# Kernel optimization log

Hardware: AMD Instinct MI355X
Metric: run time of the kernel (lower is better)

## Reference

```python
import jax, jax.numpy as jnp
import numpy as np
import math

FILTER_SIZE = 11
FILTER_SIGMA = 1.5
C1 = 0.01 ** 2
C2 = 0.03 ** 2
PAD = FILTER_SIZE // 2


def _make_gauss_kernel(sigma, kernel_size, channel=3):
    mean = np.floor(0.5 * kernel_size)
    x = np.arange(kernel_size, dtype=np.float64)
    k1d = np.exp(-((x - mean) ** 2) / (2 * sigma ** 2)) * (1.0 / (2 * math.pi * sigma ** 2))
    k2d = np.outer(k1d, k1d).astype(np.float32)
    k2d = k2d / k2d.sum()
    # OIHW depthwise kernel: [channel, 1, k, k]
    return np.broadcast_to(k2d[None, None], (channel, 1, kernel_size, kernel_size)).copy()


def _depthwise_blur(x, kernel):
    # x: [B, 3, H, W], kernel: [3, 1, k, k]; groups=3, SAME padding (k//2)
    return jax.lax.conv_general_dilated(
        x, kernel,
        window_strides=(1, 1),
        padding=[(PAD, PAD), (PAD, PAD)],
        dimension_numbers=('NCHW', 'OIHW', 'NCHW'),
        feature_group_count=3,
    )


def setup_inputs() -> dict:
    key = jax.random.key(0)
    k1, k2 = jax.random.split(key)
    B, C, H, W = 32, 3, 512, 512
    image1 = jax.random.uniform(k1, (B, C, H, W), dtype=jnp.float32)
    image2 = jax.random.uniform(k2, (B, C, H, W), dtype=jnp.float32)
    gauss_kernel = jnp.asarray(_make_gauss_kernel(FILTER_SIGMA, FILTER_SIZE, channel=3))
    return {"image1": image1, "image2": image2, "gauss_kernel": gauss_kernel}


def reference(image1, image2, gauss_kernel):
    mu1 = _depthwise_blur(image1, gauss_kernel)
    mu2 = _depthwise_blur(image2, gauss_kernel)
    mu1_sq = mu1 * mu1
    mu2_sq = mu2 * mu2
    mu1_mu2 = mu1 * mu2
    sig1_sq = _depthwise_blur(image1 * image1, gauss_kernel) - mu1_sq
    sig2_sq = _depthwise_blur(image2 * image2, gauss_kernel) - mu2_sq
    sig1_sig2 = _depthwise_blur(image1 * image2, gauss_kernel) - mu1_mu2
    ssim_num = (2.0 * mu1_mu2 + C1) * (2.0 * sig1_sig2 + C2)
    ssim_den = (mu1_sq + mu2_sq + C1) * (sig1_sq + sig2_sq + C2)
    ssim_map = ssim_num / ssim_den
    dssim_map = (1.0 - ssim_map) * 0.5
    return dssim_map.mean()  # size_average=True
```

## Files before the change

kernel.cpp:

```cpp
#include <hip/hip_runtime.h>
#include <math.h>


namespace {
constexpr int IMG = 512;
constexpr int TW = 32;
constexpr int RB = 32;
constexpr int RING = RB + 10;
constexpr int SLOT = 44;
constexpr int XGN = TW / 8;
constexpr int SEGR = 128;
constexpr int NCHUNK = SEGR / RB;
constexpr int SEGN = IMG / SEGR;
constexpr int CTILES = IMG / TW;
constexpr int NIMG = 96;
constexpr float C1c = 1e-4f;
constexpr float C2c = 9e-4f;
constexpr float INV_N = 1.0f / 25165824.0f;
}

typedef float v2f __attribute__((ext_vector_type(2)));

__global__ void dssim_zero(float* ws) { ws[0] = 0.0f; }

__global__ void dssim_final(const float* __restrict__ ws, float* __restrict__ out) {
  out[0] = ws[0] * INV_N;
}

__global__ __launch_bounds__(256, 4) void dssim_main(
    const float* __restrict__ im1, const float* __restrict__ im2,
    const float* __restrict__ gk, float* __restrict__ ws)
{
  __shared__ float sR[XGN * RING * SLOT];

  const int tid = threadIdx.x;
  const int bid = blockIdx.x;
  const int img = bid >> 6;
  const int rem = bid & 63;
  const int tsx = rem & 15;
  const int seg = rem >> 4;
  const int X0s = tsx * TW;
  const int Y0  = seg * SEGR;

  const float* __restrict__ p1 = im1 + (size_t)img * (IMG * IMG);
  const float* __restrict__ p2 = im2 + (size_t)img * (IMG * IMG);

  float wt[11];
  {
    float ic = 1.0f / sqrtf(gk[5 * 11 + 5]);
    #pragma unroll
    for (int i = 0; i < 11; ++i) wt[i] = gk[i * 11 + 5] * ic;
  }
  v2f wp[12];
  #pragma unroll
  for (int m = 0; m < 12; ++m) {
    float lo = (m <= 10) ? wt[m] : 0.f;
    float hi = (m >= 1) ? wt[m - 1] : 0.f;
    wp[m].x = lo; wp[m].y = hi;
  }

  const int c   = tid & 31;
  const int yg  = tid >> 5;
  const int xg3 = c >> 3;
  const int cl  = c & 7;

  float lsum = 0.f;

  for (int kc = 0; kc < NCHUNK; ++kc) {
    const int r0    = (kc == 0) ? -5 : RB * kc + 5;
    const int ntask = (kc == 0) ? 8 * RING : 8 * RB;
    for (int t = tid; t < ntask; t += 256) {
      const int colsub = t & 7;
      const int dr  = t >> 3;
      const int rl  = r0 + dr;
      const int ry  = Y0 + rl;
      const int rr  = (rl + 5) % RING;
      const int xg  = colsub >> 1;
      const int sub = colsub & 1;
      const int cbs = X0s + xg * 8 + sub * 4 - 8;

      float a20[20], b20[20];
      if ((unsigned)ry < (unsigned)IMG) {
        const float* row1 = p1 + (size_t)ry * IMG;
        const float* row2 = p2 + (size_t)ry * IMG;
        if (cbs >= 0 && cbs + 20 <= IMG) {
          #pragma unroll
          for (int i = 0; i < 5; ++i) {
            float4 v1 = *(const float4*)(row1 + cbs + 4 * i);
            float4 v2 = *(const float4*)(row2 + cbs + 4 * i);
            a20[4*i+0] = v1.x; a20[4*i+1] = v1.y; a20[4*i+2] = v1.z; a20[4*i+3] = v1.w;
            b20[4*i+0] = v2.x; b20[4*i+1] = v2.y; b20[4*i+2] = v2.z; b20[4*i+3] = v2.w;
          }
        } else {
          #pragma unroll
          for (int e = 0; e < 20; ++e) {
            int cc = cbs + e;
            bool ok = (unsigned)cc < (unsigned)IMG;
            a20[e] = ok ? row1[cc] : 0.f;
            b20[e] = ok ? row2[cc] : 0.f;
          }
        }
      } else {
        #pragma unroll
        for (int e = 0; e < 20; ++e) { a20[e] = 0.f; b20[e] = 0.f; }
      }

      v2f o0[2], o1[2], o2[2], o3[2], o4[2];
      #pragma unroll
      for (int jp = 0; jp < 2; ++jp) {
        o0[jp] = 0.f; o1[jp] = 0.f; o2[jp] = 0.f; o3[jp] = 0.f; o4[jp] = 0.f;
      }
      #pragma unroll
      for (int i = 3; i <= 16; ++i) {
        float va = a20[i], vb = b20[i];
        float pa = va * va, pb = vb * vb, pab = va * vb;
        v2f va2; va2.x = va; va2.y = va;
        v2f vb2; vb2.x = vb; vb2.y = vb;
        v2f pa2; pa2.x = pa; pa2.y = pa;
        v2f pb2; pb2.x = pb; pb2.y = pb;
        v2f pc2; pc2.x = pab; pc2.y = pab;
        if (i - 3 < 12) {
          v2f w = wp[i - 3];
          o0[0] = __builtin_elementwise_fma(w, va2, o0[0]);
          o1[0] = __builtin_elementwise_fma(w, vb2, o1[0]);
          o2[0] = __builtin_elementwise_fma(w, pa2, o2[0]);
          o3[0] = __builtin_elementwise_fma(w, pb2, o3[0]);
          o4[0] = __builtin_elementwise_fma(w, pc2, o4[0]);
        }
        if (i - 5 >= 0) {
          v2f w = wp[i - 5];
          o0[1] = __builtin_elementwise_fma(w, va2, o0[1]);
          o1[1] = __builtin_elementwise_fma(w, vb2, o1[1]);
          o2[1] = __builtin_elementwise_fma(w, pa2, o2[1]);
          o3[1] = __builtin_elementwise_fma(w, pb2, o3[1]);
          o4[1] = __builtin_elementwise_fma(w, pc2, o4[1]);
        }
      }

      const int base  = (xg * RING + rr) * SLOT;
      const int jbase = base + 16 * sub;
      *(float4*)&sR[jbase]      = make_float4(o0[0].x, o1[0].x, o2[0].x, o3[0].x);
      *(float4*)&sR[jbase + 4]  = make_float4(o0[0].y, o1[0].y, o2[0].y, o3[0].y);
      *(float4*)&sR[jbase + 8]  = make_float4(o0[1].x, o1[1].x, o2[1].x, o3[1].x);
      *(float4*)&sR[jbase + 12] = make_float4(o0[1].y, o1[1].y, o2[1].y, o3[1].y);
      *(float4*)&sR[base + 32 + 4 * sub] =
          make_float4(o4[0].x, o4[0].y, o4[1].x, o4[1].y);
    }
    __syncthreads();

    v2f m1p[2], m2p[2], e11p[2], e22p[2], e12p[2];
    #pragma unroll
    for (int jp = 0; jp < 2; ++jp) {
      m1p[jp] = 0.f; m2p[jp] = 0.f; e11p[jp] = 0.f; e22p[jp] = 0.f; e12p[jp] = 0.f;
    }

    const int y0l = RB * kc + yg * 4;
    int idx = y0l % RING;
    #pragma unroll
    for (int rr = 0; rr < 14; ++rr) {
      const int a = (xg3 * RING + idx) * SLOT;
      float4 v4 = *(const float4*)&sR[a + 4 * cl];
      float  v5 = sR[a + 32 + cl];
      v2f x1; x1.x = v4.x; x1.y = v4.x;
      v2f x2; x2.x = v4.y; x2.y = v4.y;
      v2f x3; x3.x = v4.z; x3.y = v4.z;
      v2f x4; x4.x = v4.w; x4.y = v4.w;
      v2f x5; x5.x = v5;   x5.y = v5;
      if (rr < 12) {
        v2f w = wp[rr];
        m1p[0]  = __builtin_elementwise_fma(w, x1, m1p[0]);
        m2p[0]  = __builtin_elementwise_fma(w, x2, m2p[0]);
        e11p[0] = __builtin_elementwise_fma(w, x3, e11p[0]);
        e22p[0] = __builtin_elementwise_fma(w, x4, e22p[0]);
        e12p[0] = __builtin_elementwise_fma(w, x5, e12p[0]);
      }
      if (rr >= 2) {
        v2f w = wp[rr - 2];
        m1p[1]  = __builtin_elementwise_fma(w, x1, m1p[1]);
        m2p[1]  = __builtin_elementwise_fma(w, x2, m2p[1]);
        e11p[1] = __builtin_elementwise_fma(w, x3, e11p[1]);
        e22p[1] = __builtin_elementwise_fma(w, x4, e22p[1]);
        e12p[1] = __builtin_elementwise_fma(w, x5, e12p[1]);
      }
      idx++; if (idx == RING) idx = 0;
    }

    #pragma unroll
    for (int jp = 0; jp < 2; ++jp) {
      v2f m1 = m1p[jp], m2 = m2p[jp];
      v2f m1s = m1 * m1, m2s = m2 * m2, m12 = m1 * m2;
      v2f s11 = e11p[jp] - m1s, s22 = e22p[jp] - m2s, s12 = e12p[jp] - m12;
      v2f num = (2.f * m12 + C1c) * (2.f * s12 + C2c);
      v2f den = (m1s + m2s + C1c) * (s11 + s22 + C2c);
      lsum += (1.f - num.x * __builtin_amdgcn_rcpf(den.x)) * 0.5f;
      lsum += (1.f - num.y * __builtin_amdgcn_rcpf(den.y)) * 0.5f;
    }
    __syncthreads();
  }

  #pragma unroll
  for (int off = 32; off > 0; off >>= 1) lsum += __shfl_down(lsum, off);
  if ((tid & 63) == 0) sR[tid >> 6] = lsum;
  __syncthreads();
  if (tid == 0) atomicAdd(ws, sR[0] + sR[1] + sR[2] + sR[3]);
}

extern "C" void kernel_launch(void* const* d_in, const int* in_sizes, int n_in,
                              void* d_out, int out_size, void* d_ws, size_t ws_size,
                              hipStream_t stream) {
  const float* im1 = (const float*)d_in[0];
  const float* im2 = (const float*)d_in[1];
  const float* gk  = (const float*)d_in[2];
  float* out = (float*)d_out;
  float* ws  = (float*)d_ws;

  hipLaunchKernelGGL(dssim_zero, dim3(1), dim3(1), 0, stream, ws);
  hipLaunchKernelGGL(dssim_main, dim3(NIMG * CTILES * SEGN), dim3(256), 0, stream,
                     im1, im2, gk, ws);
  hipLaunchKernelGGL(dssim_final, dim3(1), dim3(1), 0, stream, ws, out);
}
```

Measured before the change: 284.5 us.

## Merge squared-moment blurs into one channel and swizzle shared-memory slots

```diff
diff --git a/kernel.cpp b/kernel.cpp
--- a/kernel.cpp
+++ b/kernel.cpp
@@ -7,7 +7,7 @@
 constexpr int TW = 32;
 constexpr int RB = 32;
 constexpr int RING = RB + 10;
-constexpr int SLOT = 44;
+constexpr int SLOT = 40;
 constexpr int XGN = TW / 8;
 constexpr int SEGR = 128;
 constexpr int NCHUNK = SEGR / RB;
@@ -105,82 +105,80 @@
         for (int e = 0; e < 20; ++e) { a20[e] = 0.f; b20[e] = 0.f; }
       }
 
-      v2f o0[2], o1[2], o2[2], o3[2], o4[2];
+      v2f o0[2], o1[2], oS[2], oX[2];
       #pragma unroll
       for (int jp = 0; jp < 2; ++jp) {
-        o0[jp] = 0.f; o1[jp] = 0.f; o2[jp] = 0.f; o3[jp] = 0.f; o4[jp] = 0.f;
+        o0[jp] = 0.f; o1[jp] = 0.f; oS[jp] = 0.f; oX[jp] = 0.f;
       }
       #pragma unroll
       for (int i = 3; i <= 16; ++i) {
         float va = a20[i], vb = b20[i];
-        float pa = va * va, pb = vb * vb, pab = va * vb;
+        float px = va * vb;
+        float ps = va * va + vb * vb;
         v2f va2; va2.x = va; va2.y = va;
         v2f vb2; vb2.x = vb; vb2.y = vb;
-        v2f pa2; pa2.x = pa; pa2.y = pa;
-        v2f pb2; pb2.x = pb; pb2.y = pb;
-        v2f pc2; pc2.x = pab; pc2.y = pab;
+        v2f ps2; ps2.x = ps; ps2.y = ps;
+        v2f px2; px2.x = px; px2.y = px;
         if (i - 3 < 12) {
           v2f w = wp[i - 3];
           o0[0] = __builtin_elementwise_fma(w, va2, o0[0]);
           o1[0] = __builtin_elementwise_fma(w, vb2, o1[0]);
-          o2[0] = __builtin_elementwise_fma(w, pa2, o2[0]);
-          o3[0] = __builtin_elementwise_fma(w, pb2, o3[0]);
-          o4[0] = __builtin_elementwise_fma(w, pc2, o4[0]);
+          oS[0] = __builtin_elementwise_fma(w, ps2, oS[0]);
+          oX[0] = __builtin_elementwise_fma(w, px2, oX[0]);
         }
         if (i - 5 >= 0) {
           v2f w = wp[i - 5];
           o0[1] = __builtin_elementwise_fma(w, va2, o0[1]);
           o1[1] = __builtin_elementwise_fma(w, vb2, o1[1]);
-          o2[1] = __builtin_elementwise_fma(w, pa2, o2[1]);
-          o3[1] = __builtin_elementwise_fma(w, pb2, o3[1]);
-          o4[1] = __builtin_elementwise_fma(w, pc2, o4[1]);
+          oS[1] = __builtin_elementwise_fma(w, ps2, oS[1]);
+          oX[1] = __builtin_elementwise_fma(w, px2, oX[1]);
         }
       }
 
-      const int base  = (xg * RING + rr) * SLOT;
-      const int jbase = base + 16 * sub;
-      *(float4*)&sR[jbase]      = make_float4(o0[0].x, o1[0].x, o2[0].x, o3[0].x);
-      *(float4*)&sR[jbase + 4]  = make_float4(o0[0].y, o1[0].y, o2[0].y, o3[0].y);
-      *(float4*)&sR[jbase + 8]  = make_float4(o0[1].x, o1[1].x, o2[1].x, o3[1].x);
-      *(float4*)&sR[jbase + 12] = make_float4(o0[1].y, o1[1].y, o2[1].y, o3[1].y);
-      *(float4*)&sR[base + 32 + 4 * sub] =
-          make_float4(o4[0].x, o4[0].y, o4[1].x, o4[1].y);
+      const int base = (xg * RING + rr) * SLOT;
+      const int rot  = 4 * (rr & 7) + 20 * xg;
+      const int q0   = 4 * sub;
+      *(float4*)&sR[base + ((4 * (q0 + 0) + rot) & 31)] =
+          make_float4(o0[0].x, o1[0].x, oS[0].x, oX[0].x);
+      *(float4*)&sR[base + ((4 * (q0 + 1) + rot) & 31)] =
+          make_float4(o0[0].y, o1[0].y, oS[0].y, oX[0].y);
+      *(float4*)&sR[base + ((4 * (q0 + 2) + rot) & 31)] =
+          make_float4(o0[1].x, o1[1].x, oS[1].x, oX[1].x);
+      *(float4*)&sR[base + ((4 * (q0 + 3) + rot) & 31)] =
+          make_float4(o0[1].y, o1[1].y, oS[1].y, oX[1].y);
     }
     __syncthreads();
 
-    v2f m1p[2], m2p[2], e11p[2], e22p[2], e12p[2];
+    v2f m1p[2], m2p[2], eSp[2], eXp[2];
     #pragma unroll
     for (int jp = 0; jp < 2; ++jp) {
-      m1p[jp] = 0.f; m2p[jp] = 0.f; e11p[jp] = 0.f; e22p[jp] = 0.f; e12p[jp] = 0.f;
+      m1p[jp] = 0.f; m2p[jp] = 0.f; eSp[jp] = 0.f; eXp[jp] = 0.f;
     }
 
     const int y0l = RB * kc + yg * 4;
     int idx = y0l % RING;
     #pragma unroll
     for (int rr = 0; rr < 14; ++rr) {
-      const int a = (xg3 * RING + idx) * SLOT;
-      float4 v4 = *(const float4*)&sR[a + 4 * cl];
-      float  v5 = sR[a + 32 + cl];
+      const int a = (xg3 * RING + idx) * SLOT +
+                    ((4 * cl + 4 * (idx & 7) + 20 * xg3) & 31);
+      float4 v4 = *(const float4*)&sR[a];
       v2f x1; x1.x = v4.x; x1.y = v4.x;
       v2f x2; x2.x = v4.y; x2.y = v4.y;
       v2f x3; x3.x = v4.z; x3.y = v4.z;
       v2f x4; x4.x = v4.w; x4.y = v4.w;
-      v2f x5; x5.x = v5;   x5.y = v5;
       if (rr < 12) {
         v2f w = wp[rr];
-        m1p[0]  = __builtin_elementwise_fma(w, x1, m1p[0]);
-        m2p[0]  = __builtin_elementwise_fma(w, x2, m2p[0]);
-        e11p[0] = __builtin_elementwise_fma(w, x3, e11p[0]);
-        e22p[0] = __builtin_elementwise_fma(w, x4, e22p[0]);
-        e12p[0] = __builtin_elementwise_fma(w, x5, e12p[0]);
+        m1p[0] = __builtin_elementwise_fma(w, x1, m1p[0]);
+        m2p[0] = __builtin_elementwise_fma(w, x2, m2p[0]);
+        eSp[0] = __builtin_elementwise_fma(w, x3, eSp[0]);
+        eXp[0] = __builtin_elementwise_fma(w, x4, eXp[0]);
       }
       if (rr >= 2) {
         v2f w = wp[rr - 2];
-        m1p[1]  = __builtin_elementwise_fma(w, x1, m1p[1]);
-        m2p[1]  = __builtin_elementwise_fma(w, x2, m2p[1]);
-        e11p[1] = __builtin_elementwise_fma(w, x3, e11p[1]);
-        e22p[1] = __builtin_elementwise_fma(w, x4, e22p[1]);
-        e12p[1] = __builtin_elementwise_fma(w, x5, e12p[1]);
+        m1p[1] = __builtin_elementwise_fma(w, x1, m1p[1]);
+        m2p[1] = __builtin_elementwise_fma(w, x2, m2p[1]);
+        eSp[1] = __builtin_elementwise_fma(w, x3, eSp[1]);
+        eXp[1] = __builtin_elementwise_fma(w, x4, eXp[1]);
       }
       idx++; if (idx == RING) idx = 0;
     }
@@ -189,9 +187,10 @@
     for (int jp = 0; jp < 2; ++jp) {
       v2f m1 = m1p[jp], m2 = m2p[jp];
       v2f m1s = m1 * m1, m2s = m2 * m2, m12 = m1 * m2;
-      v2f s11 = e11p[jp] - m1s, s22 = e22p[jp] - m2s, s12 = e12p[jp] - m12;
+      v2f sS  = eSp[jp] - m1s - m2s;
+      v2f s12 = eXp[jp] - m12;
       v2f num = (2.f * m12 + C1c) * (2.f * s12 + C2c);
-      v2f den = (m1s + m2s + C1c) * (s11 + s22 + C2c);
+      v2f den = (m1s + m2s + C1c) * (sS + C2c);
       lsum += (1.f - num.x * __builtin_amdgcn_rcpf(den.x)) * 0.5f;
       lsum += (1.f - num.y * __builtin_amdgcn_rcpf(den.y)) * 0.5f;
     }
```

New measurement: 280.2 us. Within noise of the previous version (-1.5%).
